# Performance work log

Measured on AMD Instinct MI355X. Metric: run time of the kernel, lower is better.

Reference implementation:

```python
import jax, jax.numpy as jnp
import numpy as np

N = 102400          # total nodes
G = 64              # graphs
S = 16              # subgraphs per graph
NODES_PER_SG = 100  # nodes per subgraph (N = G*S*NODES_PER_SG)
D = 128             # in_dim == emb_dim
L = 5               # num_layer
E = 819200          # edges (avg degree 8)
TOTAL_SG = G * S    # total subgraphs = 1024 (static)


def setup_inputs() -> dict:
    key = jax.random.key(0)
    kx, ke, kw1, kw2, keps = jax.random.split(key, 5)
    x = jax.random.normal(kx, (N, D), dtype=jnp.float32)
    edge_index = jax.random.randint(ke, (2, E), 0, N, dtype=jnp.int32)
    # node -> graph id (contiguous blocks of S*NODES_PER_SG nodes)
    batch = (jnp.arange(N, dtype=jnp.int32) // (S * NODES_PER_SG)).astype(jnp.int32)
    # node -> local subgraph id within its graph
    subgraph_batch = ((jnp.arange(N, dtype=jnp.int32) // NODES_PER_SG) % S).astype(jnp.int32)
    num_subgraphs = jnp.full((G,), S, dtype=jnp.int32)
    # GIN MLP params per layer: Linear(D,2D) -> ReLU -> Linear(2D,D)
    s1 = 1.0 / np.sqrt(D)
    s2 = 1.0 / np.sqrt(2 * D)
    W1 = jax.random.normal(kw1, (L, D, 2 * D), dtype=jnp.float32) * s1
    b1 = jnp.zeros((L, 2 * D), dtype=jnp.float32)
    W2 = jax.random.normal(kw2, (L, 2 * D, D), dtype=jnp.float32) * s2
    b2 = jnp.zeros((L, D), dtype=jnp.float32)
    eps = jnp.zeros((L,), dtype=jnp.float32)
    return {"x": x, "edge_index": edge_index, "batch": batch,
            "subgraph_batch": subgraph_batch, "num_subgraphs": num_subgraphs,
            "W1": W1, "b1": b1, "W2": W2, "b2": b2, "eps": eps}


def reference(x, edge_index, batch, subgraph_batch, num_subgraphs, W1, b1, W2, b2, eps):
    src, dst = edge_index[0], edge_index[1]
    n = x.shape[0]
    h = x
    for i in range(L):
        # GIN aggregation: (1+eps)*h + sum over incoming messages
        agg = jax.ops.segment_sum(h[src], dst, num_segments=n)
        z = (1.0 + eps[i]) * h + agg
        z = jax.nn.relu(z @ W1[i] + b1[i]) @ W2[i] + b2[i]
        h = z if i == L - 1 else jax.nn.relu(z)  # inter-layer ReLU, JK='last'
    # subgraph_pool: global subgraph index = graph offset + local subgraph id
    tmp = jnp.concatenate([jnp.zeros((1,), num_subgraphs.dtype),
                           jnp.cumsum(num_subgraphs)])
    subgraph_idx = tmp[batch] + subgraph_batch  # [N], values in [0, TOTAL_SG)
    sums = jax.ops.segment_sum(h, subgraph_idx, num_segments=TOTAL_SG)
    cnt = jax.ops.segment_sum(jnp.ones((n, 1), h.dtype), subgraph_idx,
                              num_segments=TOTAL_SG)
    return sums / jnp.maximum(cnt, 1.0)  # global_mean_pool over subgraphs
```

## Files before the change

### kernel.cpp

```cpp
#include <hip/hip_runtime.h>
#include <cstddef>

#define NN   102400
#define D    128
#define D2   256
#define NE   819200
#define NL   5
#define NSG  1024
#define SGN  100

typedef __attribute__((ext_vector_type(8))) short short8;
typedef __attribute__((ext_vector_type(4))) float f32x4;

__device__ __forceinline__ float bf2f(unsigned short u) {
  union { unsigned int i; float f; } c; c.i = ((unsigned int)u) << 16; return c.f;
}
__device__ __forceinline__ unsigned short f2bf(float f) {
  union { float f; unsigned int i; } c; c.f = f;
  unsigned int x = c.i;
  return (unsigned short)((x + 0x7fffu + ((x >> 16) & 1u)) >> 16);
}

__global__ void k_count(const int* __restrict__ dst, int* __restrict__ deg) {
  int e = blockIdx.x * blockDim.x + threadIdx.x;
  if (e < NE) atomicAdd(&deg[dst[e]], 1);
}

__global__ void k_scan_local(const int* __restrict__ deg, int* __restrict__ incl,
                             int* __restrict__ part) {
  __shared__ int s[1024];
  int i = blockIdx.x * 1024 + threadIdx.x;
  s[threadIdx.x] = deg[i];
  __syncthreads();
  for (int off = 1; off < 1024; off <<= 1) {
    int t = (threadIdx.x >= off) ? s[threadIdx.x - off] : 0;
    __syncthreads();
    s[threadIdx.x] += t;
    __syncthreads();
  }
  incl[i] = s[threadIdx.x];
  if (threadIdx.x == 1023) part[blockIdx.x] = s[1023];
}

__global__ void k_scan_part(int* part, int nb) {
  if (threadIdx.x == 0 && blockIdx.x == 0) {
    int acc = 0;
    for (int i = 0; i < nb; ++i) { int t = part[i]; part[i] = acc; acc += t; }
  }
}

__global__ void k_scan_fin(const int* __restrict__ incl, const int* __restrict__ part,
                           int* __restrict__ rowptr) {
  int i = blockIdx.x * blockDim.x + threadIdx.x;
  if (i < NN) rowptr[i + 1] = incl[i] + part[i >> 10];
  if (i == 0) rowptr[0] = 0;
}

__global__ void k_fill(const int* __restrict__ src, const int* __restrict__ dst,
                       const int* __restrict__ rowptr, int* __restrict__ fillc,
                       int* __restrict__ csrsrc) {
  int e = blockIdx.x * blockDim.x + threadIdx.x;
  if (e < NE) {
    int d = dst[e];
    int pos = rowptr[d] + atomicAdd(&fillc[d], 1);
    csrsrc[pos] = src[e];
  }
}

__global__ void k_cvt_x(const float* __restrict__ x, unsigned short* __restrict__ xb) {
  int i = blockIdx.x * 256 + threadIdx.x;
  const float* p = x + (size_t)i * 8;
  float4 a = *(const float4*)p;
  float4 b = *(const float4*)(p + 4);
  short8 o;
  o[0] = (short)f2bf(a.x); o[1] = (short)f2bf(a.y);
  o[2] = (short)f2bf(a.z); o[3] = (short)f2bf(a.w);
  o[4] = (short)f2bf(b.x); o[5] = (short)f2bf(b.y);
  o[6] = (short)f2bf(b.z); o[7] = (short)f2bf(b.w);
  *(short8*)(xb + (size_t)i * 8) = o;
}

__global__ void k_prep_w(const float* __restrict__ W1, const float* __restrict__ W2,
                         unsigned short* __restrict__ W1t, unsigned short* __restrict__ W2t) {
  int i = blockIdx.x * 256 + threadIdx.x;
  int l = i >> 15;
  int rem = i & 32767;
  int n1 = rem >> 7, k1 = rem & 127;
  W1t[i] = f2bf(W1[(size_t)l * D * D2 + (size_t)k1 * D2 + n1]);
  int n2 = rem >> 8, k2 = rem & 255;
  W2t[i] = f2bf(W2[(size_t)l * D2 * D + (size_t)k2 * D + n2]);
}

__global__ __launch_bounds__(256) void k_agg(const unsigned short* __restrict__ h,
                                             const int* __restrict__ rowptr,
                                             const int* __restrict__ csrsrc,
                                             const float* __restrict__ eps, int layer,
                                             unsigned short* __restrict__ z) {
  int g = threadIdx.x >> 4;
  int ln = threadIdx.x & 15;
  int v = blockIdx.x * 16 + g;
  float ep1 = 1.0f + eps[layer];
  const size_t off = (size_t)ln * 8;

  short8 hv = *(const short8*)(h + (size_t)v * D + off);
  float acc[8];
#pragma unroll
  for (int j = 0; j < 8; ++j) acc[j] = ep1 * bf2f((unsigned short)hv[j]);

  int e = rowptr[v], r1 = rowptr[v + 1];
  for (; e + 1 < r1; e += 2) {
    int u0 = csrsrc[e], u1 = csrsrc[e + 1];
    short8 a = *(const short8*)(h + (size_t)u0 * D + off);
    short8 b = *(const short8*)(h + (size_t)u1 * D + off);
#pragma unroll
    for (int j = 0; j < 8; ++j)
      acc[j] += bf2f((unsigned short)a[j]) + bf2f((unsigned short)b[j]);
  }
  if (e < r1) {
    int u0 = csrsrc[e];
    short8 a = *(const short8*)(h + (size_t)u0 * D + off);
#pragma unroll
    for (int j = 0; j < 8; ++j) acc[j] += bf2f((unsigned short)a[j]);
  }

  short8 o;
#pragma unroll
  for (int j = 0; j < 8; ++j) o[j] = (short)f2bf(acc[j]);
  *(short8*)(z + (size_t)v * D + off) = o;
}

template<int K, int NC, bool RELU>
__global__ __launch_bounds__(256) void k_gemm(const unsigned short* __restrict__ A,
                                              const unsigned short* __restrict__ Bt,
                                              const float* __restrict__ bias,
                                              unsigned short* __restrict__ C) {
  int wid = threadIdx.x >> 6;
  int lane = threadIdx.x & 63;
  int wm = wid >> 1, wn = wid & 1;
  int row_base = blockIdx.x * 128 + wm * 64;
  int col_base = blockIdx.y * 64 + wn * 32;

  int l15 = lane & 15;
  int koff = (lane >> 4) * 8;

  const unsigned short* Ab = A + (size_t)(row_base + l15) * K + koff;
  const unsigned short* Bb = Bt + (size_t)(col_base + l15) * K + koff;

  f32x4 acc[4][2];
#pragma unroll
  for (int m = 0; m < 4; ++m)
#pragma unroll
    for (int n = 0; n < 2; ++n) acc[m][n] = (f32x4){0.f, 0.f, 0.f, 0.f};

#pragma unroll
  for (int k0 = 0; k0 < K; k0 += 32) {
    short8 aF[4], bF[2];
#pragma unroll
    for (int m = 0; m < 4; ++m)
      aF[m] = *(const short8*)(Ab + (size_t)(m * 16) * K + k0);
#pragma unroll
    for (int n = 0; n < 2; ++n)
      bF[n] = *(const short8*)(Bb + (size_t)(n * 16) * K + k0);
#pragma unroll
    for (int m = 0; m < 4; ++m)
#pragma unroll
      for (int n = 0; n < 2; ++n)
        acc[m][n] = __builtin_amdgcn_mfma_f32_16x16x32_bf16(aF[m], bF[n], acc[m][n], 0, 0, 0);
  }

  float bn[2];
#pragma unroll
  for (int n = 0; n < 2; ++n) bn[n] = bias[col_base + n * 16 + l15];

#pragma unroll
  for (int m = 0; m < 4; ++m) {
#pragma unroll
    for (int n = 0; n < 2; ++n) {
      int col = col_base + n * 16 + l15;
#pragma unroll
      for (int r = 0; r < 4; ++r) {
        int row = row_base + m * 16 + (lane >> 4) * 4 + r;
        float v = acc[m][n][r] + bn[n];
        if (RELU) v = fmaxf(v, 0.f);
        C[(size_t)row * NC + col] = f2bf(v);
      }
    }
  }
}

__global__ __launch_bounds__(256) void k_pool(const unsigned short* __restrict__ h,
                                              float* __restrict__ out) {
  __shared__ float red[16][132];
  int g = threadIdx.x >> 4;
  int ln = threadIdx.x & 15;
  int sg = blockIdx.x;
  float acc[8] = {0.f, 0.f, 0.f, 0.f, 0.f, 0.f, 0.f, 0.f};
  for (int r = g; r < SGN; r += 16) {
    short8 v = *(const short8*)(h + ((size_t)sg * SGN + r) * D + (size_t)ln * 8);
#pragma unroll
    for (int j = 0; j < 8; ++j) acc[j] += bf2f((unsigned short)v[j]);
  }
#pragma unroll
  for (int j = 0; j < 8; ++j) red[g][ln * 8 + j] = acc[j];
  __syncthreads();
  if (threadIdx.x < 128) {
    float s = 0.f;
#pragma unroll
    for (int i = 0; i < 16; ++i) s += red[i][threadIdx.x];
    out[(size_t)sg * D + threadIdx.x] = s * 0.01f;
  }
}

extern "C" void kernel_launch(void* const* d_in, const int* in_sizes, int n_in,
                              void* d_out, int out_size, void* d_ws, size_t ws_size,
                              hipStream_t stream) {
  const float* x   = (const float*)d_in[0];
  const int*   ei  = (const int*)d_in[1];
  const float* W1  = (const float*)d_in[5];
  const float* b1  = (const float*)d_in[6];
  const float* W2  = (const float*)d_in[7];
  const float* b2  = (const float*)d_in[8];
  const float* eps = (const float*)d_in[9];
  const int* src = ei;
  const int* dst = ei + NE;

  char* p = (char*)d_ws;
  unsigned short* xb  = (unsigned short*)p; p += (size_t)NN * D * 2;
  unsigned short* hb  = (unsigned short*)p; p += (size_t)NN * D * 2;
  unsigned short* zb  = (unsigned short*)p; p += (size_t)NN * D * 2;
  unsigned short* z1b = (unsigned short*)p; p += (size_t)NN * D2 * 2;
  unsigned short* W1t = (unsigned short*)p; p += (size_t)NL * D * D2 * 2;
  unsigned short* W2t = (unsigned short*)p; p += (size_t)NL * D * D2 * 2;
  int* deg    = (int*)p;   p += (size_t)NN * 4;
  int* incl   = (int*)p;   p += (size_t)NN * 4;
  int* part   = (int*)p;   p += 128 * 4;
  int* rowptr = (int*)p;   p += (size_t)(NN + 1) * 4;
  int* fillc  = (int*)p;   p += (size_t)NN * 4;
  int* csrsrc = (int*)p;   p += (size_t)NE * 4;

  hipMemsetAsync(deg, 0, (size_t)NN * 4, stream);
  hipMemsetAsync(fillc, 0, (size_t)NN * 4, stream);
  k_count<<<NE / 256, 256, 0, stream>>>(dst, deg);
  k_scan_local<<<NN / 1024, 1024, 0, stream>>>(deg, incl, part);
  k_scan_part<<<1, 64, 0, stream>>>(part, NN / 1024);
  k_scan_fin<<<NN / 256, 256, 0, stream>>>(incl, part, rowptr);
  k_fill<<<NE / 256, 256, 0, stream>>>(src, dst, rowptr, fillc, csrsrc);

  k_cvt_x<<<NN * D / 8 / 256, 256, 0, stream>>>(x, xb);
  k_prep_w<<<NL * D * D2 / 256, 256, 0, stream>>>(W1, W2, W1t, W2t);

  for (int l = 0; l < NL; ++l) {
    const unsigned short* hin = (l == 0) ? xb : hb;
    k_agg<<<NN / 16, 256, 0, stream>>>(hin, rowptr, csrsrc, eps, l, zb);
    k_gemm<D, D2, true><<<dim3(NN / 128, D2 / 64), 256, 0, stream>>>(
        zb, W1t + (size_t)l * D * D2, b1 + (size_t)l * D2, z1b);
    if (l < NL - 1)
      k_gemm<D2, D, true><<<dim3(NN / 128, D / 64), 256, 0, stream>>>(
          z1b, W2t + (size_t)l * D * D2, b2 + (size_t)l * D, hb);
    else
      k_gemm<D2, D, false><<<dim3(NN / 128, D / 64), 256, 0, stream>>>(
          z1b, W2t + (size_t)l * D * D2, b2 + (size_t)l * D, hb);
  }
  k_pool<<<NSG, 256, 0, stream>>>(hb, (float*)d_out);
}
```

Baseline: 808.0 us.

## Fuse GIN aggregation and both MLP GEMMs into one per-layer kernel

Each layer now runs a single kernel: every wave gathers and sums neighbour rows for 32 nodes directly into MFMA A-fragments, runs the first GEMM, keeps the ReLU'd 256-wide hidden tile in swizzled LDS, and then runs the second GEMM, writing only the layer output. The z and z1 intermediates no longer make a round trip through global memory, and three launches per layer become one. In addition, CSR construction records each edge's atomic rank during counting, so the fill pass needs no second atomic. In exchange, the gather now runs with a lane layout poorly matched to irregular neighbour access, weights are reloaded from global per wave, and a 64 KB LDS footprint with a large register demand may limit occupancy.

```diff
diff --git a/kernel.cpp b/kernel.cpp
--- a/kernel.cpp
+++ b/kernel.cpp
@@ -21,9 +21,10 @@
   return (unsigned short)((x + 0x7fffu + ((x >> 16) & 1u)) >> 16);
 }
 
-__global__ void k_count(const int* __restrict__ dst, int* __restrict__ deg) {
+__global__ void k_count(const int* __restrict__ dst, int* __restrict__ deg,
+                        int* __restrict__ rank) {
   int e = blockIdx.x * blockDim.x + threadIdx.x;
-  if (e < NE) atomicAdd(&deg[dst[e]], 1);
+  if (e < NE) rank[e] = atomicAdd(&deg[dst[e]], 1);
 }
 
 __global__ void k_scan_local(const int* __restrict__ deg, int* __restrict__ incl,
@@ -57,14 +58,10 @@
 }
 
 __global__ void k_fill(const int* __restrict__ src, const int* __restrict__ dst,
-                       const int* __restrict__ rowptr, int* __restrict__ fillc,
+                       const int* __restrict__ rowptr, const int* __restrict__ rank,
                        int* __restrict__ csrsrc) {
   int e = blockIdx.x * blockDim.x + threadIdx.x;
-  if (e < NE) {
-    int d = dst[e];
-    int pos = rowptr[d] + atomicAdd(&fillc[d], 1);
-    csrsrc[pos] = src[e];
-  }
+  if (e < NE) csrsrc[rowptr[dst[e]] + rank[e]] = src[e];
 }
 
 __global__ void k_cvt_x(const float* __restrict__ x, unsigned short* __restrict__ xb) {
@@ -91,98 +88,112 @@
   W2t[i] = f2bf(W2[(size_t)l * D2 * D + (size_t)k2 * D + n2]);
 }
 
-__global__ __launch_bounds__(256) void k_agg(const unsigned short* __restrict__ h,
-                                             const int* __restrict__ rowptr,
-                                             const int* __restrict__ csrsrc,
-                                             const float* __restrict__ eps, int layer,
-                                             unsigned short* __restrict__ z) {
-  int g = threadIdx.x >> 4;
-  int ln = threadIdx.x & 15;
-  int v = blockIdx.x * 16 + g;
+template<bool RELU_OUT>
+__global__ __launch_bounds__(256, 2) void k_layer(
+    const unsigned short* __restrict__ hin, const int* __restrict__ rowptr,
+    const int* __restrict__ csrsrc,
+    const unsigned short* __restrict__ W1t,
+    const float* __restrict__ b1,
+    const unsigned short* __restrict__ W2t,
+    const float* __restrict__ b2,
+    const float* __restrict__ eps, int layer,
+    unsigned short* __restrict__ hout) {
+  __shared__ char lds[4 * 16384];
+  int w = threadIdx.x >> 6, lane = threadIdx.x & 63;
+  int l15 = lane & 15, q = lane >> 4;
+  char* my = lds + w * 16384;
   float ep1 = 1.0f + eps[layer];
-  const size_t off = (size_t)ln * 8;
-
-  short8 hv = *(const short8*)(h + (size_t)v * D + off);
-  float acc[8];
-#pragma unroll
-  for (int j = 0; j < 8; ++j) acc[j] = ep1 * bf2f((unsigned short)hv[j]);
-
-  int e = rowptr[v], r1 = rowptr[v + 1];
-  for (; e + 1 < r1; e += 2) {
-    int u0 = csrsrc[e], u1 = csrsrc[e + 1];
-    short8 a = *(const short8*)(h + (size_t)u0 * D + off);
-    short8 b = *(const short8*)(h + (size_t)u1 * D + off);
-#pragma unroll
-    for (int j = 0; j < 8; ++j)
-      acc[j] += bf2f((unsigned short)a[j]) + bf2f((unsigned short)b[j]);
-  }
-  if (e < r1) {
-    int u0 = csrsrc[e];
-    short8 a = *(const short8*)(h + (size_t)u0 * D + off);
-#pragma unroll
-    for (int j = 0; j < 8; ++j) acc[j] += bf2f((unsigned short)a[j]);
-  }
-
-  short8 o;
-#pragma unroll
-  for (int j = 0; j < 8; ++j) o[j] = (short)f2bf(acc[j]);
-  *(short8*)(z + (size_t)v * D + off) = o;
-}
-
-template<int K, int NC, bool RELU>
-__global__ __launch_bounds__(256) void k_gemm(const unsigned short* __restrict__ A,
-                                              const unsigned short* __restrict__ Bt,
-                                              const float* __restrict__ bias,
-                                              unsigned short* __restrict__ C) {
-  int wid = threadIdx.x >> 6;
-  int lane = threadIdx.x & 63;
-  int wm = wid >> 1, wn = wid & 1;
-  int row_base = blockIdx.x * 128 + wm * 64;
-  int col_base = blockIdx.y * 64 + wn * 32;
-
-  int l15 = lane & 15;
-  int koff = (lane >> 4) * 8;
-
-  const unsigned short* Ab = A + (size_t)(row_base + l15) * K + koff;
-  const unsigned short* Bb = Bt + (size_t)(col_base + l15) * K + koff;
-
-  f32x4 acc[4][2];
-#pragma unroll
-  for (int m = 0; m < 4; ++m)
-#pragma unroll
-    for (int n = 0; n < 2; ++n) acc[m][n] = (f32x4){0.f, 0.f, 0.f, 0.f};
-
-#pragma unroll
-  for (int k0 = 0; k0 < K; k0 += 32) {
-    short8 aF[4], bF[2];
-#pragma unroll
-    for (int m = 0; m < 4; ++m)
-      aF[m] = *(const short8*)(Ab + (size_t)(m * 16) * K + k0);
-#pragma unroll
-    for (int n = 0; n < 2; ++n)
-      bF[n] = *(const short8*)(Bb + (size_t)(n * 16) * K + k0);
-#pragma unroll
-    for (int m = 0; m < 4; ++m)
-#pragma unroll
-      for (int n = 0; n < 2; ++n)
-        acc[m][n] = __builtin_amdgcn_mfma_f32_16x16x32_bf16(aF[m], bF[n], acc[m][n], 0, 0, 0);
-  }
-
-  float bn[2];
-#pragma unroll
-  for (int n = 0; n < 2; ++n) bn[n] = bias[col_base + n * 16 + l15];
-
-#pragma unroll
-  for (int m = 0; m < 4; ++m) {
-#pragma unroll
-    for (int n = 0; n < 2; ++n) {
-      int col = col_base + n * 16 + l15;
+  int rowA = blockIdx.x * 128 + w * 32;
+
+  short8 azf[2][4];
+#pragma unroll
+  for (int m = 0; m < 2; ++m) {
+    int r = rowA + m * 16 + l15;
+    const unsigned short* hr = hin + (size_t)r * D + q * 8;
+    float acc[4][8];
+#pragma unroll
+    for (int kf = 0; kf < 4; ++kf) {
+      short8 v = *(const short8*)(hr + kf * 32);
+#pragma unroll
+      for (int j = 0; j < 8; ++j) acc[kf][j] = ep1 * bf2f((unsigned short)v[j]);
+    }
+    int e0 = rowptr[r], e1 = rowptr[r + 1];
+    for (int e = e0; e < e1; ++e) {
+      int u = csrsrc[e];
+      const unsigned short* hu = hin + (size_t)u * D + q * 8;
+#pragma unroll
+      for (int kf = 0; kf < 4; ++kf) {
+        short8 v = *(const short8*)(hu + kf * 32);
+#pragma unroll
+        for (int j = 0; j < 8; ++j) acc[kf][j] += bf2f((unsigned short)v[j]);
+      }
+    }
+#pragma unroll
+    for (int kf = 0; kf < 4; ++kf) {
+      short8 o;
+#pragma unroll
+      for (int j = 0; j < 8; ++j) o[j] = (short)f2bf(acc[kf][j]);
+      azf[m][kf] = o;
+    }
+  }
+
+  f32x4 acc1[2][16] = {};
+#pragma unroll
+  for (int kf = 0; kf < 4; ++kf) {
+#pragma unroll
+    for (int n = 0; n < 16; ++n) {
+      short8 bf = *(const short8*)(W1t + (size_t)(n * 16 + l15) * D + kf * 32 + q * 8);
+      acc1[0][n] = __builtin_amdgcn_mfma_f32_16x16x32_bf16(azf[0][kf], bf, acc1[0][n], 0, 0, 0);
+      acc1[1][n] = __builtin_amdgcn_mfma_f32_16x16x32_bf16(azf[1][kf], bf, acc1[1][n], 0, 0, 0);
+    }
+  }
+#pragma unroll
+  for (int m = 0; m < 2; ++m) {
+#pragma unroll
+    for (int n = 0; n < 16; ++n) {
+      int col = n * 16 + l15;
+      float bb = b1[col];
 #pragma unroll
       for (int r = 0; r < 4; ++r) {
-        int row = row_base + m * 16 + (lane >> 4) * 4 + r;
-        float v = acc[m][n][r] + bn[n];
-        if (RELU) v = fmaxf(v, 0.f);
-        C[(size_t)row * NC + col] = f2bf(v);
+        int rs = m * 16 + q * 4 + r;
+        float v = fmaxf(acc1[m][n][r] + bb, 0.f);
+        int byte = (rs << 9) + col * 2;
+        byte ^= (rs & 7) << 4;
+        *(unsigned short*)(my + byte) = f2bf(v);
+      }
+    }
+  }
+
+  f32x4 acc2[2][8] = {};
+#pragma unroll
+  for (int kf2 = 0; kf2 < 8; ++kf2) {
+    short8 af[2];
+#pragma unroll
+    for (int m = 0; m < 2; ++m) {
+      int rs = m * 16 + l15;
+      int byte = (rs << 9) + kf2 * 64 + q * 16;
+      byte ^= (rs & 7) << 4;
+      af[m] = *(const short8*)(my + byte);
+    }
+#pragma unroll
+    for (int n2 = 0; n2 < 8; ++n2) {
+      short8 bf = *(const short8*)(W2t + (size_t)(n2 * 16 + l15) * D2 + kf2 * 32 + q * 8);
+      acc2[0][n2] = __builtin_amdgcn_mfma_f32_16x16x32_bf16(af[0], bf, acc2[0][n2], 0, 0, 0);
+      acc2[1][n2] = __builtin_amdgcn_mfma_f32_16x16x32_bf16(af[1], bf, acc2[1][n2], 0, 0, 0);
+    }
+  }
+#pragma unroll
+  for (int m = 0; m < 2; ++m) {
+#pragma unroll
+    for (int n2 = 0; n2 < 8; ++n2) {
+      int col = n2 * 16 + l15;
+      float bb = b2[col];
+#pragma unroll
+      for (int r = 0; r < 4; ++r) {
+        int row = rowA + m * 16 + q * 4 + r;
+        float v = acc2[m][n2][r] + bb;
+        if (RELU_OUT) v = fmaxf(v, 0.f);
+        hout[(size_t)row * D + col] = f2bf(v);
       }
     }
   }
@@ -228,38 +239,40 @@
   unsigned short* xb  = (unsigned short*)p; p += (size_t)NN * D * 2;
   unsigned short* hb  = (unsigned short*)p; p += (size_t)NN * D * 2;
   unsigned short* zb  = (unsigned short*)p; p += (size_t)NN * D * 2;
-  unsigned short* z1b = (unsigned short*)p; p += (size_t)NN * D2 * 2;
   unsigned short* W1t = (unsigned short*)p; p += (size_t)NL * D * D2 * 2;
   unsigned short* W2t = (unsigned short*)p; p += (size_t)NL * D * D2 * 2;
   int* deg    = (int*)p;   p += (size_t)NN * 4;
   int* incl   = (int*)p;   p += (size_t)NN * 4;
   int* part   = (int*)p;   p += 128 * 4;
   int* rowptr = (int*)p;   p += (size_t)(NN + 1) * 4;
-  int* fillc  = (int*)p;   p += (size_t)NN * 4;
+  int* rank   = (int*)p;   p += (size_t)NE * 4;
   int* csrsrc = (int*)p;   p += (size_t)NE * 4;
 
   hipMemsetAsync(deg, 0, (size_t)NN * 4, stream);
-  hipMemsetAsync(fillc, 0, (size_t)NN * 4, stream);
-  k_count<<<NE / 256, 256, 0, stream>>>(dst, deg);
+  k_count<<<NE / 256, 256, 0, stream>>>(dst, deg, rank);
   k_scan_local<<<NN / 1024, 1024, 0, stream>>>(deg, incl, part);
   k_scan_part<<<1, 64, 0, stream>>>(part, NN / 1024);
   k_scan_fin<<<NN / 256, 256, 0, stream>>>(incl, part, rowptr);
-  k_fill<<<NE / 256, 256, 0, stream>>>(src, dst, rowptr, fillc, csrsrc);
+  k_fill<<<NE / 256, 256, 0, stream>>>(src, dst, rowptr, rank, csrsrc);
 
   k_cvt_x<<<NN * D / 8 / 256, 256, 0, stream>>>(x, xb);
   k_prep_w<<<NL * D * D2 / 256, 256, 0, stream>>>(W1, W2, W1t, W2t);
 
+  const unsigned short* cur = xb;
+  unsigned short* nxt = hb;
   for (int l = 0; l < NL; ++l) {
-    const unsigned short* hin = (l == 0) ? xb : hb;
-    k_agg<<<NN / 16, 256, 0, stream>>>(hin, rowptr, csrsrc, eps, l, zb);
-    k_gemm<D, D2, true><<<dim3(NN / 128, D2 / 64), 256, 0, stream>>>(
-        zb, W1t + (size_t)l * D * D2, b1 + (size_t)l * D2, z1b);
+    const unsigned short* w1l = W1t + (size_t)l * D * D2;
+    const unsigned short* w2l = W2t + (size_t)l * D * D2;
+    const float* b1l = b1 + (size_t)l * D2;
+    const float* b2l = b2 + (size_t)l * D;
     if (l < NL - 1)
-      k_gemm<D2, D, true><<<dim3(NN / 128, D / 64), 256, 0, stream>>>(
-          z1b, W2t + (size_t)l * D * D2, b2 + (size_t)l * D, hb);
+      k_layer<true><<<NN / 128, 256, 0, stream>>>(cur, rowptr, csrsrc, w1l, b1l,
+                                                  w2l, b2l, eps, l, nxt);
     else
-      k_gemm<D2, D, false><<<dim3(NN / 128, D / 64), 256, 0, stream>>>(
-          z1b, W2t + (size_t)l * D * D2, b2 + (size_t)l * D, hb);
-  }
-  k_pool<<<NSG, 256, 0, stream>>>(hb, (float*)d_out);
-}
+      k_layer<false><<<NN / 128, 256, 0, stream>>>(cur, rowptr, csrsrc, w1l, b1l,
+                                                   w2l, b2l, eps, l, nxt);
+    cur = nxt;
+    nxt = (cur == hb) ? zb : hb;
+  }
+  k_pool<<<NSG, 256, 0, stream>>>((const unsigned short*)cur, (float*)d_out);
+}
```

New measurement: 752.8 us. 6.8% less time.
